# Performance work log

Hardware: AMD Instinct MI355X
Metric: run time of the kernel (lower is better)

Reference implementation:

```python
import jax, jax.numpy as jnp
import numpy as np

N, IN_DIM, H, D, A = 50000, 256, 8, 32, 8
E = 800000
CLAMP = 5.0
EPS = 1e-16


def setup_inputs() -> dict:
    key = jax.random.key(0)
    ks = jax.random.split(key, 12)
    d = H * D
    inp = {
        "x": jax.random.normal(ks[0], (N, IN_DIM), jnp.float32),
        "node_rotation_angles": jax.random.normal(ks[1], (N, A), jnp.float32),
        "edge_index": jax.random.randint(ks[2], (2, E), 0, N, jnp.int32),
        # Linear params stored as [in, out] for x @ W + b
        "Wq": jax.random.normal(ks[3], (IN_DIM, d), jnp.float32) * 0.02,
        "bq": jnp.zeros((d,), jnp.float32),
        "Wk": jax.random.normal(ks[4], (IN_DIM, d), jnp.float32) * 0.02,
        "bk": jnp.zeros((d,), jnp.float32),
        "Wv": jax.random.normal(ks[5], (IN_DIM, d), jnp.float32) * 0.02,
        "bv": jnp.zeros((d,), jnp.float32),
        "S": jax.random.normal(ks[6], (A, d // 2), jnp.float32) * 0.02,
    }
    return inp


def _rotate_half(t):
    # torch.stack([-t[...,1::2], t[...,::2]], dim=2).reshape(t.shape)
    # == concat of (-odd half, even half) along last dim
    return jnp.concatenate([-t[..., 1::2], t[..., ::2]], axis=-1)


def reference(x, node_rotation_angles, edge_index, Wq, bq, Wk, bk, Wv, bv, S):
    Q = (x @ Wq + bq).reshape(-1, H, D)   # [N,H,D]
    K = (x @ Wk + bk).reshape(-1, H, D)
    V = (x @ Wv + bv).reshape(-1, H, D)

    # learned rotation angles: [N,A] @ softmax(S over d/2) -> [N, d/2]
    thetas = node_rotation_angles @ jax.nn.softmax(S, axis=1)
    thetas = jnp.repeat(thetas, 2, axis=1).reshape(-1, H, D)  # repeat_interleave(2)
    cos_p, sin_p = jnp.cos(thetas), jnp.sin(thetas)
    Q = Q * cos_p + _rotate_half(Q) * sin_p
    K = K * cos_p + _rotate_half(K) * sin_p

    src, dst = edge_index[0], edge_index[1]
    # per-edge scores: gather K[src], Q[dst], dot over D
    score = jnp.einsum("ehd,ehd->eh", K[src], Q[dst]) / jnp.sqrt(jnp.float32(D))
    score = jnp.clip(score, -CLAMP, CLAMP)  # [E,H]

    # scatter softmax grouped by destination node
    smax = jax.ops.segment_max(score, dst, num_segments=N)      # [N,H]
    ex = jnp.exp(score - smax[dst])
    den = jax.ops.segment_sum(ex, dst, num_segments=N)          # [N,H]
    attn = ex / (den[dst] + EPS)                                 # [E,H]

    # weighted scatter-add aggregation
    msg = V[src] * attn[:, :, None]                              # [E,H,D]
    wV = jax.ops.segment_sum(msg, dst, num_segments=N)           # [N,H,D]
    return wV
```

## Files before the change

### kernel.cpp

```cpp
#include <hip/hip_runtime.h>
#include <math.h>

#define NN      50000
#define IND     256
#define HH      8
#define DD      32
#define DMODEL  256
#define AA      8
#define EE      800000
#define HALF    128

#define P_OFF    0
#define QB_OFF   1024
#define KB_OFF   (QB_OFF + NN*DMODEL/2)
#define V_OFF    (KB_OFF + NN*DMODEL/2)
#define INT_OFF  (V_OFF + NN*DMODEL)
#define CNT_I    0
#define OFF_I    (CNT_I + NN)
#define CUR_I    (OFF_I + NN + 1)
#define PSRC_I   (CUR_I + NN)
#define INT_TOTAL (PSRC_I + EE)
#define WTH_OFF  (INT_OFF + INT_TOTAL + 3)
#define WTL_OFF  (WTH_OFF + (768*256)/2)

typedef __attribute__((ext_vector_type(8))) short short8v;
typedef __attribute__((ext_vector_type(4))) float f32x4;

__device__ __forceinline__ unsigned short f2bf(float f) {
    union { float f; unsigned u; } v; v.f = f;
    unsigned r = v.u + 0x7fffu + ((v.u >> 16) & 1u);
    return (unsigned short)(r >> 16);
}
__device__ __forceinline__ float bf2f(unsigned short h) {
    union { unsigned u; float f; } v; v.u = ((unsigned)h) << 16;
    return v.f;
}

__global__ __launch_bounds__(512) void softmax_S(const float* __restrict__ S,
                                                 float* __restrict__ P) {
    const int wave = threadIdx.x >> 6;
    const int lane = threadIdx.x & 63;
    const float* row = S + wave * HALF;
    float s0 = row[lane], s1 = row[lane + 64];
    float m = fmaxf(s0, s1);
    #pragma unroll
    for (int off = 32; off; off >>= 1) m = fmaxf(m, __shfl_xor(m, off));
    float e0 = expf(s0 - m), e1 = expf(s1 - m);
    float sum = e0 + e1;
    #pragma unroll
    for (int off = 32; off; off >>= 1) sum += __shfl_xor(sum, off);
    float inv = 1.0f / sum;
    P[wave * HALF + lane]      = e0 * inv;
    P[wave * HALF + lane + 64] = e1 * inv;
}

__global__ __launch_bounds__(256) void split_wt(const float* __restrict__ Wq,
                                                const float* __restrict__ Wk,
                                                const float* __restrict__ Wv,
                                                short* __restrict__ wt_hi,
                                                short* __restrict__ wt_lo) {
    const int g = blockIdx.x;
    const int k = threadIdx.x;
    const int m = g >> 8, c = g & 255;
    const float* W = (m == 0) ? Wq : (m == 1) ? Wk : Wv;
    const float v = W[k * 256 + c];
    const unsigned short hi = f2bf(v);
    wt_hi[g * 256 + k] = (short)hi;
    wt_lo[g * 256 + k] = (short)f2bf(v - bf2f(hi));
}

__global__ __launch_bounds__(256) void qkv_mfma(
    const float* __restrict__ x,
    const short* __restrict__ wt_hi, const short* __restrict__ wt_lo,
    const float* __restrict__ bq, const float* __restrict__ bk,
    const float* __restrict__ bv,
    unsigned short* __restrict__ Qb, unsigned short* __restrict__ Kb,
    float* __restrict__ V) {
    __shared__ short Ahi[64 * 40], Alo[64 * 40];
    __shared__ short Bhi[192 * 40], Blo[192 * 40];
    const int t = threadIdx.x;
    const int w = t >> 6, l = t & 63;
    const int lr = l & 15, kg = l >> 4;
    const int n0 = blockIdx.x * 64;
    const int by = blockIdx.y;

    f32x4 zero = 0.0f;
    f32x4 acc[12];
    #pragma unroll
    for (int i = 0; i < 12; ++i) acc[i] = zero;

    const int arow = t >> 2;
    const int ak8  = (t & 3) << 3;
    const bool aok = (n0 + arow) < NN;
    const float* xrow = x + (size_t)(n0 + arow) * IND + ak8;
    const int bcol = t >> 2;

    for (int ks = 0; ks < 8; ++ks) {
        const int k0 = ks * 32;
        float av[8];
        if (aok) {
            const float4 u0 = *(const float4*)(xrow + k0);
            const float4 u1 = *(const float4*)(xrow + k0 + 4);
            av[0] = u0.x; av[1] = u0.y; av[2] = u0.z; av[3] = u0.w;
            av[4] = u1.x; av[5] = u1.y; av[6] = u1.z; av[7] = u1.w;
        } else {
            #pragma unroll
            for (int i = 0; i < 8; ++i) av[i] = 0.f;
        }
        short8v ahi, alo;
        #pragma unroll
        for (int i = 0; i < 8; ++i) {
            const unsigned short h = f2bf(av[i]);
            ahi[i] = (short)h;
            alo[i] = (short)f2bf(av[i] - bf2f(h));
        }
        short8v bh[3], bl[3];
        #pragma unroll
        for (int rep = 0; rep < 3; ++rep) {
            const int g = by * 192 + rep * 64 + bcol;
            bh[rep] = *(const short8v*)&wt_hi[(size_t)g * 256 + k0 + ak8];
            bl[rep] = *(const short8v*)&wt_lo[(size_t)g * 256 + k0 + ak8];
        }
        __syncthreads();
        *(short8v*)&Ahi[arow * 40 + ak8] = ahi;
        *(short8v*)&Alo[arow * 40 + ak8] = alo;
        #pragma unroll
        for (int rep = 0; rep < 3; ++rep) {
            *(short8v*)&Bhi[(rep * 64 + bcol) * 40 + ak8] = bh[rep];
            *(short8v*)&Blo[(rep * 64 + bcol) * 40 + ak8] = bl[rep];
        }
        __syncthreads();
        const short8v a_hi = *(const short8v*)&Ahi[(w * 16 + lr) * 40 + kg * 8];
        const short8v a_lo = *(const short8v*)&Alo[(w * 16 + lr) * 40 + kg * 8];
        #pragma unroll
        for (int ct = 0; ct < 12; ++ct) {
            const short8v b_hi = *(const short8v*)&Bhi[(ct * 16 + lr) * 40 + kg * 8];
            const short8v b_lo = *(const short8v*)&Blo[(ct * 16 + lr) * 40 + kg * 8];
            acc[ct] = __builtin_amdgcn_mfma_f32_16x16x32_bf16(a_hi, b_hi, acc[ct], 0, 0, 0);
            acc[ct] = __builtin_amdgcn_mfma_f32_16x16x32_bf16(a_lo, b_hi, acc[ct], 0, 0, 0);
            acc[ct] = __builtin_amdgcn_mfma_f32_16x16x32_bf16(a_hi, b_lo, acc[ct], 0, 0, 0);
        }
    }
    #pragma unroll
    for (int ct = 0; ct < 12; ++ct) {
        const int g = by * 192 + ct * 16 + lr;
        const int m = g >> 8, c = g & 255;
        const float bb = ((m == 0) ? bq : (m == 1) ? bk : bv)[c];
        #pragma unroll
        for (int r = 0; r < 4; ++r) {
            const int n = n0 + w * 16 + kg * 4 + r;
            if (n < NN) {
                const float val = acc[ct][r] + bb;
                if (m == 0)      Qb[(size_t)n * 256 + c] = f2bf(val);
                else if (m == 1) Kb[(size_t)n * 256 + c] = f2bf(val);
                else             V [(size_t)n * 256 + c] = val;
            }
        }
    }
}

__global__ __launch_bounds__(256) void rotate_qk(unsigned short* __restrict__ Qb,
                                                 unsigned short* __restrict__ Kb,
                                                 const float* __restrict__ ang,
                                                 const float* __restrict__ P) {
    __shared__ float cbuf[HALF], sbuf[HALF];
    const int n = blockIdx.x;
    const int t = threadIdx.x;
    if (t < HALF) {
        float th = 0.f;
        #pragma unroll
        for (int a = 0; a < AA; ++a) th = fmaf(ang[n * AA + a], P[a * HALF + t], th);
        cbuf[t] = cosf(th);
        sbuf[t] = sinf(th);
    }
    __syncthreads();
    const int hd = t & 31;
    const int rowb = n * DMODEL;
    const int headb = t & ~31;
    const int pl = (hd < 16) ? (headb + 2 * hd + 1) : (headb + 2 * (hd - 16));
    const float sgn = (hd < 16) ? -1.f : 1.f;
    const float c = cbuf[t >> 1], s = sbuf[t >> 1];
    const float qv = bf2f(Qb[rowb + t]), qp = bf2f(Qb[rowb + pl]);
    const float kv = bf2f(Kb[rowb + t]), kp = bf2f(Kb[rowb + pl]);
    __syncthreads();
    Qb[rowb + t] = f2bf(fmaf(qv, c, sgn * qp * s));
    Kb[rowb + t] = f2bf(fmaf(kv, c, sgn * kp * s));
}

__global__ __launch_bounds__(256) void hist(const int* __restrict__ ei,
                                            int* __restrict__ cnt) {
    const unsigned e = blockIdx.x * 256u + threadIdx.x;
    if (e < EE) atomicAdd(&cnt[ei[EE + e]], 1);
}

__global__ __launch_bounds__(1024) void scan_offsets(const int* __restrict__ cnt,
                                                     int* __restrict__ off,
                                                     int* __restrict__ cursor) {
    __shared__ int wsum[16];
    __shared__ int chunk_base;
    const int t = threadIdx.x;
    const int wave = t >> 6, lane = t & 63;
    if (t == 0) chunk_base = 0;
    __syncthreads();
    for (int base = 0; base < NN; base += 1024) {
        const int i = base + t;
        const int v = (i < NN) ? cnt[i] : 0;
        int s = v;
        #pragma unroll
        for (int o = 1; o < 64; o <<= 1) {
            int u = __shfl_up(s, o);
            if (lane >= o) s += u;
        }
        if (lane == 63) wsum[wave] = s;
        __syncthreads();
        if (wave == 0 && lane < 16) {
            int ss = wsum[lane];
            #pragma unroll
            for (int o = 1; o < 16; o <<= 1) {
                int u = __shfl_up(ss, o);
                if (lane >= o) ss += u;
            }
            wsum[lane] = ss;
        }
        __syncthreads();
        const int waveoff = (wave == 0) ? 0 : wsum[wave - 1];
        const int excl = chunk_base + waveoff + s - v;
        if (i < NN) { off[i] = excl; cursor[i] = excl; }
        __syncthreads();
        if (t == 0) chunk_base += wsum[15];
        __syncthreads();
    }
    if (t == 0) off[NN] = EE;
}

__global__ __launch_bounds__(256) void scatter(const int* __restrict__ ei,
                                               int* __restrict__ cursor,
                                               int* __restrict__ psrc) {
    const unsigned e = blockIdx.x * 256u + threadIdx.x;
    if (e < EE) {
        const int dst = ei[EE + e];
        const int pos = atomicAdd(&cursor[dst], 1);
        psrc[pos] = ei[e];
    }
}

__global__ __launch_bounds__(256) void agg_csr(const unsigned short* __restrict__ Qb,
                                               const unsigned short* __restrict__ Kb,
                                               const float* __restrict__ V,
                                               const int* __restrict__ off,
                                               const int* __restrict__ psrc,
                                               float* __restrict__ out) {
    const unsigned gid = blockIdx.x * 256u + threadIdx.x;
    const int n = gid >> 6;
    const int r = gid & 63;
    const ushort4 qu = *(const ushort4*)(Qb + (size_t)n * DMODEL + r * 4);
    const float qs = 0.17677669529663687f;
    const float qx = bf2f(qu.x) * qs, qy = bf2f(qu.y) * qs;
    const float qz = bf2f(qu.z) * qs, qw = bf2f(qu.w) * qs;
    float4 acc = make_float4(0.f, 0.f, 0.f, 0.f);
    float wsum = 0.f;
    const int j0 = off[n], j1 = off[n + 1];
    for (int base = j0; base < j1; base += 64) {
        const int m = j1 - base < 64 ? j1 - base : 64;
        const int sv = (base + r < j1) ? psrc[base + r] : 0;
        for (int i = 0; i < m; ++i) {
            const int src = __shfl(sv, i);
            const ushort4 ku = *(const ushort4*)(Kb + (size_t)src * DMODEL + r * 4);
            float p = bf2f(ku.x) * qx;
            p = fmaf(bf2f(ku.y), qy, p);
            p = fmaf(bf2f(ku.z), qz, p);
            p = fmaf(bf2f(ku.w), qw, p);
            p += __shfl_xor(p, 1);
            p += __shfl_xor(p, 2);
            p += __shfl_xor(p, 4);
            float sc = fminf(fmaxf(p, -5.f), 5.f);
            const float wv = expf(sc);
            const float4 v4 = *(const float4*)(V + (size_t)src * DMODEL + r * 4);
            acc.x = fmaf(wv, v4.x, acc.x);
            acc.y = fmaf(wv, v4.y, acc.y);
            acc.z = fmaf(wv, v4.z, acc.z);
            acc.w = fmaf(wv, v4.w, acc.w);
            wsum += wv;
        }
    }
    const float inv = 1.0f / (wsum + 1e-16f);
    float4 o;
    o.x = acc.x * inv; o.y = acc.y * inv; o.z = acc.z * inv; o.w = acc.w * inv;
    *(float4*)(out + (size_t)n * DMODEL + r * 4) = o;
}

extern "C" void kernel_launch(void* const* d_in, const int* in_sizes, int n_in,
                              void* d_out, int out_size, void* d_ws, size_t ws_size,
                              hipStream_t stream) {
    (void)in_sizes; (void)n_in; (void)out_size; (void)ws_size;
    const float* x    = (const float*)d_in[0];
    const float* ang  = (const float*)d_in[1];
    const int*   ei   = (const int*)d_in[2];
    const float* Wq   = (const float*)d_in[3];
    const float* bq   = (const float*)d_in[4];
    const float* Wk   = (const float*)d_in[5];
    const float* bk   = (const float*)d_in[6];
    const float* Wv   = (const float*)d_in[7];
    const float* bv   = (const float*)d_in[8];
    const float* S    = (const float*)d_in[9];
    float* out = (float*)d_out;
    float* ws  = (float*)d_ws;

    float* P = ws + P_OFF;
    unsigned short* Qb = (unsigned short*)(ws + QB_OFF);
    unsigned short* Kb = (unsigned short*)(ws + KB_OFF);
    float* V = ws + V_OFF;
    int* iws    = (int*)(ws + INT_OFF);
    int* cnt    = iws + CNT_I;
    int* off    = iws + OFF_I;
    int* cursor = iws + CUR_I;
    int* psrc   = iws + PSRC_I;
    short* wt_hi = (short*)(ws + WTH_OFF);
    short* wt_lo = (short*)(ws + WTL_OFF);

    hipMemsetAsync(cnt, 0, (size_t)NN * sizeof(int), stream);

    softmax_S<<<1, 512, 0, stream>>>(S, P);

    split_wt<<<768, 256, 0, stream>>>(Wq, Wk, Wv, wt_hi, wt_lo);

    dim3 ggrid((NN + 63) / 64, 4);
    qkv_mfma<<<ggrid, 256, 0, stream>>>(x, wt_hi, wt_lo, bq, bk, bv, Qb, Kb, V);

    rotate_qk<<<NN, 256, 0, stream>>>(Qb, Kb, ang, P);

    hist<<<(EE + 255) / 256, 256, 0, stream>>>(ei, cnt);
    scan_offsets<<<1, 1024, 0, stream>>>(cnt, off, cursor);
    scatter<<<(EE + 255) / 256, 256, 0, stream>>>(ei, cursor, psrc);

    agg_csr<<<(NN * 64) / 256, 256, 0, stream>>>(Qb, Kb, V, off, psrc, out);
}
```

Before: 568.9 us.

## Store V as bf16, vectorize rotation per head, unroll edge loop by two

```diff
diff --git a/kernel.cpp b/kernel.cpp
--- a/kernel.cpp
+++ b/kernel.cpp
@@ -24,6 +24,7 @@
 #define WTL_OFF  (WTH_OFF + (768*256)/2)
 
 typedef __attribute__((ext_vector_type(8))) short short8v;
+typedef __attribute__((ext_vector_type(8))) unsigned short us8v;
 typedef __attribute__((ext_vector_type(4))) float f32x4;
 
 __device__ __forceinline__ unsigned short f2bf(float f) {
@@ -75,7 +76,7 @@
     const float* __restrict__ bq, const float* __restrict__ bk,
     const float* __restrict__ bv,
     unsigned short* __restrict__ Qb, unsigned short* __restrict__ Kb,
-    float* __restrict__ V) {
+    unsigned short* __restrict__ Vb) {
     __shared__ short Ahi[64 * 40], Alo[64 * 40];
     __shared__ short Bhi[192 * 40], Blo[192 * 40];
     const int t = threadIdx.x;
@@ -146,15 +147,11 @@
         const int g = by * 192 + ct * 16 + lr;
         const int m = g >> 8, c = g & 255;
         const float bb = ((m == 0) ? bq : (m == 1) ? bk : bv)[c];
+        unsigned short* O = (m == 0) ? Qb : (m == 1) ? Kb : Vb;
         #pragma unroll
         for (int r = 0; r < 4; ++r) {
             const int n = n0 + w * 16 + kg * 4 + r;
-            if (n < NN) {
-                const float val = acc[ct][r] + bb;
-                if (m == 0)      Qb[(size_t)n * 256 + c] = f2bf(val);
-                else if (m == 1) Kb[(size_t)n * 256 + c] = f2bf(val);
-                else             V [(size_t)n * 256 + c] = val;
-            }
+            if (n < NN) O[(size_t)n * 256 + c] = f2bf(acc[ct][r] + bb);
         }
     }
 }
@@ -163,28 +160,66 @@
                                                  unsigned short* __restrict__ Kb,
                                                  const float* __restrict__ ang,
                                                  const float* __restrict__ P) {
-    __shared__ float cbuf[HALF], sbuf[HALF];
-    const int n = blockIdx.x;
     const int t = threadIdx.x;
-    if (t < HALF) {
-        float th = 0.f;
-        #pragma unroll
-        for (int a = 0; a < AA; ++a) th = fmaf(ang[n * AA + a], P[a * HALF + t], th);
-        cbuf[t] = cosf(th);
-        sbuf[t] = sinf(th);
-    }
-    __syncthreads();
-    const int hd = t & 31;
-    const int rowb = n * DMODEL;
-    const int headb = t & ~31;
-    const int pl = (hd < 16) ? (headb + 2 * hd + 1) : (headb + 2 * (hd - 16));
-    const float sgn = (hd < 16) ? -1.f : 1.f;
-    const float c = cbuf[t >> 1], s = sbuf[t >> 1];
-    const float qv = bf2f(Qb[rowb + t]), qp = bf2f(Qb[rowb + pl]);
-    const float kv = bf2f(Kb[rowb + t]), kp = bf2f(Kb[rowb + pl]);
-    __syncthreads();
-    Qb[rowb + t] = f2bf(fmaf(qv, c, sgn * qp * s));
-    Kb[rowb + t] = f2bf(fmaf(kv, c, sgn * kp * s));
+    const int n = blockIdx.x * 32 + (t >> 3);
+    if (n >= NN) return;
+    const int h = t & 7;
+    const size_t base = (size_t)n * DMODEL + h * 32;
+
+    us8v qv[4], kv[4];
+    #pragma unroll
+    for (int i = 0; i < 4; ++i) {
+        qv[i] = *(const us8v*)(Qb + base + i * 8);
+        kv[i] = *(const us8v*)(Kb + base + i * 8);
+    }
+    float av[AA];
+    #pragma unroll
+    for (int a = 0; a < AA; ++a) av[a] = ang[n * AA + a];
+
+    float th[16];
+    #pragma unroll
+    for (int j = 0; j < 16; ++j) th[j] = 0.f;
+    #pragma unroll
+    for (int a = 0; a < AA; ++a) {
+        const float aa = av[a];
+        const float* Pr = P + a * HALF + h * 16;
+        #pragma unroll
+        for (int j4 = 0; j4 < 4; ++j4) {
+            const float4 p4 = *(const float4*)(Pr + j4 * 4);
+            th[j4 * 4 + 0] = fmaf(aa, p4.x, th[j4 * 4 + 0]);
+            th[j4 * 4 + 1] = fmaf(aa, p4.y, th[j4 * 4 + 1]);
+            th[j4 * 4 + 2] = fmaf(aa, p4.z, th[j4 * 4 + 2]);
+            th[j4 * 4 + 3] = fmaf(aa, p4.w, th[j4 * 4 + 3]);
+        }
+    }
+    float cth[16], sth[16];
+    #pragma unroll
+    for (int j = 0; j < 16; ++j) { cth[j] = cosf(th[j]); sth[j] = sinf(th[j]); }
+
+    float q[32], k[32];
+    #pragma unroll
+    for (int i = 0; i < 4; ++i) {
+        #pragma unroll
+        for (int j = 0; j < 8; ++j) {
+            q[i * 8 + j] = bf2f(qv[i][j]);
+            k[i * 8 + j] = bf2f(kv[i][j]);
+        }
+    }
+    us8v qo[4], ko[4];
+    #pragma unroll
+    for (int hd = 0; hd < 32; ++hd) {
+        const float c = cth[hd >> 1], s = sth[hd >> 1];
+        float qr, kr;
+        if (hd < 16) { qr = -q[2 * hd + 1];    kr = -k[2 * hd + 1]; }
+        else         { qr =  q[2 * (hd - 16)]; kr =  k[2 * (hd - 16)]; }
+        qo[hd >> 3][hd & 7] = f2bf(fmaf(q[hd], c, qr * s));
+        ko[hd >> 3][hd & 7] = f2bf(fmaf(k[hd], c, kr * s));
+    }
+    #pragma unroll
+    for (int i = 0; i < 4; ++i) {
+        *(us8v*)(Qb + base + i * 8) = qo[i];
+        *(us8v*)(Kb + base + i * 8) = ko[i];
+    }
 }
 
 __global__ __launch_bounds__(256) void hist(const int* __restrict__ ei,
@@ -246,7 +281,7 @@
 
 __global__ __launch_bounds__(256) void agg_csr(const unsigned short* __restrict__ Qb,
                                                const unsigned short* __restrict__ Kb,
-                                               const float* __restrict__ V,
+                                               const unsigned short* __restrict__ Vb,
                                                const int* __restrict__ off,
                                                const int* __restrict__ psrc,
                                                float* __restrict__ out) {
@@ -263,9 +298,42 @@
     for (int base = j0; base < j1; base += 64) {
         const int m = j1 - base < 64 ? j1 - base : 64;
         const int sv = (base + r < j1) ? psrc[base + r] : 0;
-        for (int i = 0; i < m; ++i) {
+        int i = 0;
+        for (; i + 1 < m; i += 2) {
+            const int src0 = __shfl(sv, i);
+            const int src1 = __shfl(sv, i + 1);
+            const ushort4 ku0 = *(const ushort4*)(Kb + (size_t)src0 * DMODEL + r * 4);
+            const ushort4 ku1 = *(const ushort4*)(Kb + (size_t)src1 * DMODEL + r * 4);
+            const ushort4 vu0 = *(const ushort4*)(Vb + (size_t)src0 * DMODEL + r * 4);
+            const ushort4 vu1 = *(const ushort4*)(Vb + (size_t)src1 * DMODEL + r * 4);
+            float p0 = bf2f(ku0.x) * qx;
+            p0 = fmaf(bf2f(ku0.y), qy, p0);
+            p0 = fmaf(bf2f(ku0.z), qz, p0);
+            p0 = fmaf(bf2f(ku0.w), qw, p0);
+            float p1 = bf2f(ku1.x) * qx;
+            p1 = fmaf(bf2f(ku1.y), qy, p1);
+            p1 = fmaf(bf2f(ku1.z), qz, p1);
+            p1 = fmaf(bf2f(ku1.w), qw, p1);
+            p0 += __shfl_xor(p0, 1);  p1 += __shfl_xor(p1, 1);
+            p0 += __shfl_xor(p0, 2);  p1 += __shfl_xor(p1, 2);
+            p0 += __shfl_xor(p0, 4);  p1 += __shfl_xor(p1, 4);
+            const float w0 = expf(fminf(fmaxf(p0, -5.f), 5.f));
+            const float w1 = expf(fminf(fmaxf(p1, -5.f), 5.f));
+            acc.x = fmaf(w0, bf2f(vu0.x), acc.x);
+            acc.y = fmaf(w0, bf2f(vu0.y), acc.y);
+            acc.z = fmaf(w0, bf2f(vu0.z), acc.z);
+            acc.w = fmaf(w0, bf2f(vu0.w), acc.w);
+            wsum += w0;
+            acc.x = fmaf(w1, bf2f(vu1.x), acc.x);
+            acc.y = fmaf(w1, bf2f(vu1.y), acc.y);
+            acc.z = fmaf(w1, bf2f(vu1.z), acc.z);
+            acc.w = fmaf(w1, bf2f(vu1.w), acc.w);
+            wsum += w1;
+        }
+        if (i < m) {
             const int src = __shfl(sv, i);
             const ushort4 ku = *(const ushort4*)(Kb + (size_t)src * DMODEL + r * 4);
+            const ushort4 vu = *(const ushort4*)(Vb + (size_t)src * DMODEL + r * 4);
             float p = bf2f(ku.x) * qx;
             p = fmaf(bf2f(ku.y), qy, p);
             p = fmaf(bf2f(ku.z), qz, p);
@@ -273,13 +341,11 @@
             p += __shfl_xor(p, 1);
             p += __shfl_xor(p, 2);
             p += __shfl_xor(p, 4);
-            float sc = fminf(fmaxf(p, -5.f), 5.f);
-            const float wv = expf(sc);
-            const float4 v4 = *(const float4*)(V + (size_t)src * DMODEL + r * 4);
-            acc.x = fmaf(wv, v4.x, acc.x);
-            acc.y = fmaf(wv, v4.y, acc.y);
-            acc.z = fmaf(wv, v4.z, acc.z);
-            acc.w = fmaf(wv, v4.w, acc.w);
+            const float wv = expf(fminf(fmaxf(p, -5.f), 5.f));
+            acc.x = fmaf(wv, bf2f(vu.x), acc.x);
+            acc.y = fmaf(wv, bf2f(vu.y), acc.y);
+            acc.z = fmaf(wv, bf2f(vu.z), acc.z);
+            acc.w = fmaf(wv, bf2f(vu.w), acc.w);
             wsum += wv;
         }
     }
@@ -309,7 +375,7 @@
     float* P = ws + P_OFF;
     unsigned short* Qb = (unsigned short*)(ws + QB_OFF);
     unsigned short* Kb = (unsigned short*)(ws + KB_OFF);
-    float* V = ws + V_OFF;
+    unsigned short* Vb = (unsigned short*)(ws + V_OFF);
     int* iws    = (int*)(ws + INT_OFF);
     int* cnt    = iws + CNT_I;
     int* off    = iws + OFF_I;
@@ -325,13 +391,13 @@
     split_wt<<<768, 256, 0, stream>>>(Wq, Wk, Wv, wt_hi, wt_lo);
 
     dim3 ggrid((NN + 63) / 64, 4);
-    qkv_mfma<<<ggrid, 256, 0, stream>>>(x, wt_hi, wt_lo, bq, bk, bv, Qb, Kb, V);
-
-    rotate_qk<<<NN, 256, 0, stream>>>(Qb, Kb, ang, P);
+    qkv_mfma<<<ggrid, 256, 0, stream>>>(x, wt_hi, wt_lo, bq, bk, bv, Qb, Kb, Vb);
+
+    rotate_qk<<<(NN + 31) / 32, 256, 0, stream>>>(Qb, Kb, ang, P);
 
     hist<<<(EE + 255) / 256, 256, 0, stream>>>(ei, cnt);
     scan_offsets<<<1, 1024, 0, stream>>>(cnt, off, cursor);
     scatter<<<(EE + 255) / 256, 256, 0, stream>>>(ei, cursor, psrc);
 
-    agg_csr<<<(NN * 64) / 256, 256, 0, stream>>>(Qb, Kb, V, off, psrc, out);
-}
+    agg_csr<<<(NN * 64) / 256, 256, 0, stream>>>(Qb, Kb, Vb, off, psrc, out);
+}
```

Result: faster. 494.9 us (-13.0%).
